# Performance work log

Hardware: AMD Instinct MI355X
Metric: run time of the kernel (lower is better)

Reference implementation:

```python
import jax, jax.numpy as jnp
import numpy as np

LEAKY_SLOPE = 0.2  # PyG GATConv default negative_slope
EPS = 1e-16


def _gat_layer(h_in, src, dst, W, a_src, a_dst, b, concat):
    # h_in: [N, Fin]; src/dst: [Etot] (self-loops included); W: [Fin, H*C]
    N = h_in.shape[0]
    H, C = a_src.shape
    h = (h_in @ W).reshape(N, H, C)                       # [N,H,C]
    al_s = jnp.sum(h * a_src, axis=-1)                    # [N,H]
    al_d = jnp.sum(h * a_dst, axis=-1)                    # [N,H]
    e = jax.nn.leaky_relu(al_s[src] + al_d[dst], LEAKY_SLOPE)  # [E,H]
    emax = jax.ops.segment_max(e, dst, num_segments=N)    # segment softmax over dst
    p = jnp.exp(e - emax[dst])
    denom = jax.ops.segment_sum(p, dst, num_segments=N)
    alpha = p / (denom[dst] + EPS)                        # [E,H]
    out = jax.ops.segment_sum(h[src] * alpha[:, :, None], dst, num_segments=N)  # [N,H,C]
    out = out.reshape(N, H * C) if concat else out.mean(axis=1)
    return out + b


def setup_inputs() -> dict:
    key = jax.random.key(0)
    ks = jax.random.split(key, 16)
    N, E, Fin, Hd, Hh = 10000, 320000, 256, 128, 4

    def glorot(k, shape, fan_in):
        return jax.random.normal(k, shape, dtype=jnp.float32) * (1.0 / np.sqrt(fan_in))

    inp = {
        "x": jax.random.normal(ks[0], (N, Fin), dtype=jnp.float32),
        "edge_index": jax.random.randint(ks[1], (2, E), 0, N, dtype=jnp.int32),
        # conv1: Fin -> Hd x Hh heads, concat
        "W1": glorot(ks[2], (Fin, Hh * Hd), Fin),
        "a1_src": glorot(ks[3], (Hh, Hd), Hd),
        "a1_dst": glorot(ks[4], (Hh, Hd), Hd),
        "b1": jnp.zeros((Hh * Hd,), jnp.float32),
        # conv2: Hh*Hd -> Hd x Hh heads, concat
        "W2": glorot(ks[5], (Hh * Hd, Hh * Hd), Hh * Hd),
        "a2_src": glorot(ks[6], (Hh, Hd), Hd),
        "a2_dst": glorot(ks[7], (Hh, Hd), Hd),
        "b2": jnp.zeros((Hh * Hd,), jnp.float32),
        # conv3: Hh*Hd -> Hd, 1 head, concat=False (mean)
        "W3": glorot(ks[8], (Hh * Hd, Hd), Hh * Hd),
        "a3_src": glorot(ks[9], (1, Hd), Hd),
        "a3_dst": glorot(ks[10], (1, Hd), Hd),
        "b3": jnp.zeros((Hd,), jnp.float32),
        # classifier: Hd -> Hd//2 -> 2
        "Wc1": glorot(ks[11], (Hd, Hd // 2), Hd),
        "bc1": jnp.zeros((Hd // 2,), jnp.float32),
        "Wc2": glorot(ks[12], (Hd // 2, 2), Hd // 2),
        "bc2": jnp.zeros((2,), jnp.float32),
    }
    return inp


def reference(x, edge_index, W1, a1_src, a1_dst, b1, W2, a2_src, a2_dst, b2,
              W3, a3_src, a3_dst, b3, Wc1, bc1, Wc2, bc2):
    N = x.shape[0]
    loops = jnp.arange(N, dtype=edge_index.dtype)
    src = jnp.concatenate([edge_index[0], loops])  # PyG adds self-loops
    dst = jnp.concatenate([edge_index[1], loops])

    h = jax.nn.elu(_gat_layer(x, src, dst, W1, a1_src, a1_dst, b1, concat=True))
    h = jax.nn.elu(_gat_layer(h, src, dst, W2, a2_src, a2_dst, b2, concat=True))
    embeddings = _gat_layer(h, src, dst, W3, a3_src, a3_dst, b3, concat=False)  # [N, 128]
    out = jax.nn.relu(embeddings @ Wc1 + bc1) @ Wc2 + bc2  # [N, 2]
    return out, embeddings
```

## Files before the change

kernel.cpp:

```cpp
#include <hip/hip_runtime.h>
#include <cstddef>

#define LEAKY 0.2f
#define EPS_DEN 1e-16f

typedef short bf8_t __attribute__((ext_vector_type(8)));
typedef float f4_t __attribute__((ext_vector_type(4)));
typedef unsigned short us4_t __attribute__((ext_vector_type(4)));
typedef unsigned short us8_t __attribute__((ext_vector_type(8)));

__device__ __forceinline__ unsigned short f2bf(float f) {
    unsigned u = __float_as_uint(f);
    unsigned r = (u + 0x7fffu + ((u >> 16) & 1u)) >> 16;
    return (unsigned short)r;
}
__device__ __forceinline__ float bf2f(unsigned short h) {
    return __uint_as_float(((unsigned)h) << 16);
}

__global__ void hist_kernel(const int* __restrict__ dst, int* __restrict__ counts, int E) {
    int i = blockIdx.x * blockDim.x + threadIdx.x;
    if (i < E) atomicAdd(&counts[dst[i]], 1);
}

__global__ void scan1_kernel(int* __restrict__ cnt, int* __restrict__ bsum, int N) {
    __shared__ int s[256];
    int t = threadIdx.x;
    int i = blockIdx.x * 256 + t;
    int v = (i < N) ? cnt[i] : 0;
    s[t] = v;
    __syncthreads();
#pragma unroll
    for (int st = 1; st < 256; st <<= 1) {
        int add = (t >= st) ? s[t - st] : 0;
        __syncthreads();
        s[t] += add;
        __syncthreads();
    }
    if (i < N) cnt[i] = s[t] - v;
    if (t == 255) bsum[blockIdx.x] = s[255];
}

__global__ void scan3b_kernel(int* __restrict__ cnt, const int* __restrict__ bsum,
                              int* __restrict__ offs, int N, int NB) {
    __shared__ int sPre[64];
    __shared__ int sTot;
    int t = threadIdx.x;
    if (t < 64) {
        int v = (t < NB) ? bsum[t] : 0;
        int inc = v;
#pragma unroll
        for (int off = 1; off < 64; off <<= 1) {
            int u = __shfl_up(inc, off);
            if (t >= off) inc += u;
        }
        sPre[t] = inc - v;
        if (t == 63) sTot = inc;
    }
    __syncthreads();
    int i = blockIdx.x * 256 + t;
    if (i < N) {
        int o = cnt[i] + sPre[blockIdx.x];
        offs[i] = o;
        cnt[i] = o;
    }
    if (blockIdx.x == 0 && t == 0) offs[N] = sTot;
}

__global__ void scatter_kernel(const int* __restrict__ src, const int* __restrict__ dst,
                               int* __restrict__ cursor, int* __restrict__ csrc, int E) {
    int i = blockIdx.x * blockDim.x + threadIdx.x;
    if (i < E) {
        int d = dst[i];
        int pos = atomicAdd(&cursor[d], 1);
        csrc[pos] = src[i];
    }
}

__global__ void split_all_kernel(
    const float* __restrict__ x, unsigned short* __restrict__ xh, unsigned short* __restrict__ xl,
    int NBX,
    const float* __restrict__ W1, unsigned short* __restrict__ w1h, unsigned short* __restrict__ w1l,
    const float* __restrict__ W2, unsigned short* __restrict__ w2h, unsigned short* __restrict__ w2l,
    const float* __restrict__ W3, unsigned short* __restrict__ w3h, unsigned short* __restrict__ w3l) {
    int b = blockIdx.x, t = threadIdx.x;
    float v;
    unsigned short* ph;
    unsigned short* pl;
    int idx;
    if (b < NBX) {
        idx = b * 256 + t;
        v = x[idx];
        ph = xh; pl = xl;
    } else if (b < NBX + 512) {
        idx = (b - NBX) * 256 + t;
        int n = idx >> 8, k = idx & 255;
        v = W1[(size_t)k * 512 + n];
        ph = w1h; pl = w1l;
    } else if (b < NBX + 512 + 1024) {
        idx = (b - NBX - 512) * 256 + t;
        int n = idx >> 9, k = idx & 511;
        v = W2[(size_t)k * 512 + n];
        ph = w2h; pl = w2l;
    } else {
        idx = (b - NBX - 1536) * 256 + t;
        int n = idx >> 9, k = idx & 511;
        v = W3[(size_t)k * 128 + n];
        ph = w3h; pl = w3l;
    }
    unsigned short hv = f2bf(v);
    ph[idx] = hv;
    pl[idx] = f2bf(v - bf2f(hv));
}

__global__ __launch_bounds__(256) void mfma_gemm128_kernel(
    const unsigned short* __restrict__ Ahi, const unsigned short* __restrict__ Alo,
    const unsigned short* __restrict__ BThi, const unsigned short* __restrict__ BTlo,
    const float* __restrict__ a_src, const float* __restrict__ a_dst,
    float* __restrict__ C, float* __restrict__ als, float* __restrict__ ald,
    int M, int N, int K) {
    constexpr int BK = 32;
    __shared__ __align__(16) unsigned short sAh[128 * BK];
    __shared__ __align__(16) unsigned short sAl[128 * BK];
    __shared__ __align__(16) unsigned short sBh[128 * BK];
    __shared__ __align__(16) unsigned short sBl[128 * BK];
    __shared__ float sAls[128][2];
    __shared__ float sAld[128][2];
    int t = threadIdx.x;
    int w = t >> 6, lane = t & 63;
    int quad = lane >> 4, low = lane & 15;
    int m0 = blockIdx.y * 128, n0 = blockIdx.x * 128;
    int wm = (w & 1) * 64, wn = (w >> 1) * 64;

    f4_t acc[4][4];
#pragma unroll
    for (int i = 0; i < 4; i++)
#pragma unroll
        for (int j = 0; j < 4; j++) acc[i][j] = (f4_t){0.f, 0.f, 0.f, 0.f};

    int srow = lane >> 2;
    int schunk = lane & 3;

    for (int k0 = 0; k0 < K; k0 += BK) {
        __syncthreads();
#pragma unroll
        for (int inst = 0; inst < 2; inst++) {
            int r = w * 32 + inst * 16 + srow;
            int gm = m0 + r;
            if (gm >= M) gm = M - 1;
            size_t goff = (size_t)gm * K + k0 + schunk * 8;
            size_t loff = (size_t)(w * 2048 + inst * 1024);
            __builtin_amdgcn_global_load_lds(
                (const __attribute__((address_space(1))) void*)(Ahi + goff),
                (__attribute__((address_space(3))) void*)((char*)sAh + loff), 16, 0, 0);
            __builtin_amdgcn_global_load_lds(
                (const __attribute__((address_space(1))) void*)(Alo + goff),
                (__attribute__((address_space(3))) void*)((char*)sAl + loff), 16, 0, 0);
        }
#pragma unroll
        for (int inst = 0; inst < 2; inst++) {
            int r = w * 32 + inst * 16 + srow;
            int gn = n0 + r;
            size_t goff = (size_t)gn * K + k0 + schunk * 8;
            size_t loff = (size_t)(w * 2048 + inst * 1024);
            __builtin_amdgcn_global_load_lds(
                (const __attribute__((address_space(1))) void*)(BThi + goff),
                (__attribute__((address_space(3))) void*)((char*)sBh + loff), 16, 0, 0);
            __builtin_amdgcn_global_load_lds(
                (const __attribute__((address_space(1))) void*)(BTlo + goff),
                (__attribute__((address_space(3))) void*)((char*)sBl + loff), 16, 0, 0);
        }
        __syncthreads();

        bf8_t afh[4], bfh[4], xx[4];
#pragma unroll
        for (int i = 0; i < 4; i++) {
            int row = wm + i * 16 + low;
            afh[i] = *(const bf8_t*)&sAh[row * BK + quad * 8];
        }
#pragma unroll
        for (int j = 0; j < 4; j++) {
            int row = wn + j * 16 + low;
            bfh[j] = *(const bf8_t*)&sBh[row * BK + quad * 8];
        }
#pragma unroll
        for (int i = 0; i < 4; i++)
#pragma unroll
            for (int j = 0; j < 4; j++)
                acc[i][j] = __builtin_amdgcn_mfma_f32_16x16x32_bf16(afh[i], bfh[j], acc[i][j], 0, 0, 0);
#pragma unroll
        for (int j = 0; j < 4; j++) {
            int row = wn + j * 16 + low;
            xx[j] = *(const bf8_t*)&sBl[row * BK + quad * 8];
        }
#pragma unroll
        for (int i = 0; i < 4; i++)
#pragma unroll
            for (int j = 0; j < 4; j++)
                acc[i][j] = __builtin_amdgcn_mfma_f32_16x16x32_bf16(afh[i], xx[j], acc[i][j], 0, 0, 0);
#pragma unroll
        for (int i = 0; i < 4; i++) {
            int row = wm + i * 16 + low;
            xx[i] = *(const bf8_t*)&sAl[row * BK + quad * 8];
        }
#pragma unroll
        for (int i = 0; i < 4; i++)
#pragma unroll
            for (int j = 0; j < 4; j++)
                acc[i][j] = __builtin_amdgcn_mfma_f32_16x16x32_bf16(xx[i], bfh[j], acc[i][j], 0, 0, 0);
    }

#pragma unroll
    for (int i = 0; i < 4; i++) {
#pragma unroll
        for (int r = 0; r < 4; r++) {
            int gm = m0 + wm + i * 16 + quad * 4 + r;
            if (gm >= M) continue;
#pragma unroll
            for (int j = 0; j < 4; j++) {
                int gn = n0 + wn + j * 16 + low;
                C[(size_t)gm * N + gn] = acc[i][j][r];
            }
        }
    }

    int hd = n0 >> 7;
    float as_[4], ad_[4];
#pragma unroll
    for (int j = 0; j < 4; j++) {
        int c = wn + j * 16 + low;
        as_[j] = a_src[hd * 128 + c];
        ad_[j] = a_dst[hd * 128 + c];
    }
    int chh = wn >> 6;
#pragma unroll
    for (int i = 0; i < 4; i++) {
#pragma unroll
        for (int r = 0; r < 4; r++) {
            float v = acc[i][0][r] * as_[0] + acc[i][1][r] * as_[1] +
                      acc[i][2][r] * as_[2] + acc[i][3][r] * as_[3];
            float vd = acc[i][0][r] * ad_[0] + acc[i][1][r] * ad_[1] +
                       acc[i][2][r] * ad_[2] + acc[i][3][r] * ad_[3];
#pragma unroll
            for (int off = 1; off < 16; off <<= 1) {
                v += __shfl_xor(v, off);
                vd += __shfl_xor(vd, off);
            }
            if (low == 0) {
                int row = wm + i * 16 + quad * 4 + r;
                sAls[row][chh] = v;
                sAld[row][chh] = vd;
            }
        }
    }
    __syncthreads();
    if (t < 128) {
        int gm = m0 + t;
        if (gm < M) {
            als[gm * 4 + hd] = sAls[t][0] + sAls[t][1];
            ald[gm * 4 + hd] = sAld[t][0] + sAld[t][1];
        }
    }
}

__global__ __launch_bounds__(256) void mfma_gemm64_kernel(
    const unsigned short* __restrict__ Ahi, const unsigned short* __restrict__ Alo,
    const unsigned short* __restrict__ BThi, const unsigned short* __restrict__ BTlo,
    const float* __restrict__ a_src, const float* __restrict__ a_dst,
    float* __restrict__ C, float* __restrict__ als, float* __restrict__ ald,
    int M, int N, int K) {
    constexpr int BK = 32;
    __shared__ __align__(16) unsigned short sAh[64 * BK];
    __shared__ __align__(16) unsigned short sAl[64 * BK];
    __shared__ __align__(16) unsigned short sBh[128 * BK];
    __shared__ __align__(16) unsigned short sBl[128 * BK];
    __shared__ float sAls[64][2];
    __shared__ float sAld[64][2];
    int t = threadIdx.x;
    int w = t >> 6, lane = t & 63;
    int quad = lane >> 4, low = lane & 15;
    int m0 = blockIdx.y * 64, n0 = blockIdx.x * 128;
    int wm = (w & 1) * 32, wn = (w >> 1) * 64;

    f4_t acc[2][4];
#pragma unroll
    for (int i = 0; i < 2; i++)
#pragma unroll
        for (int j = 0; j < 4; j++) acc[i][j] = (f4_t){0.f, 0.f, 0.f, 0.f};

    int srow = lane >> 2;
    int schunk = lane & 3;

    for (int k0 = 0; k0 < K; k0 += BK) {
        __syncthreads();
        {
            int gm = m0 + w * 16 + srow;
            if (gm >= M) gm = M - 1;
            size_t goff = (size_t)gm * K + k0 + schunk * 8;
            size_t loff = (size_t)(w * 1024);
            __builtin_amdgcn_global_load_lds(
                (const __attribute__((address_space(1))) void*)(Ahi + goff),
                (__attribute__((address_space(3))) void*)((char*)sAh + loff), 16, 0, 0);
            __builtin_amdgcn_global_load_lds(
                (const __attribute__((address_space(1))) void*)(Alo + goff),
                (__attribute__((address_space(3))) void*)((char*)sAl + loff), 16, 0, 0);
        }
#pragma unroll
        for (int inst = 0; inst < 2; inst++) {
            int gn = n0 + w * 32 + inst * 16 + srow;
            size_t goff = (size_t)gn * K + k0 + schunk * 8;
            size_t loff = (size_t)(w * 2048 + inst * 1024);
            __builtin_amdgcn_global_load_lds(
                (const __attribute__((address_space(1))) void*)(BThi + goff),
                (__attribute__((address_space(3))) void*)((char*)sBh + loff), 16, 0, 0);
            __builtin_amdgcn_global_load_lds(
                (const __attribute__((address_space(1))) void*)(BTlo + goff),
                (__attribute__((address_space(3))) void*)((char*)sBl + loff), 16, 0, 0);
        }
        __syncthreads();

        bf8_t afh[2], bfh[4], xx[4];
#pragma unroll
        for (int i = 0; i < 2; i++) {
            int row = wm + i * 16 + low;
            afh[i] = *(const bf8_t*)&sAh[row * BK + quad * 8];
        }
#pragma unroll
        for (int j = 0; j < 4; j++) {
            int row = wn + j * 16 + low;
            bfh[j] = *(const bf8_t*)&sBh[row * BK + quad * 8];
        }
#pragma unroll
        for (int i = 0; i < 2; i++)
#pragma unroll
            for (int j = 0; j < 4; j++)
                acc[i][j] = __builtin_amdgcn_mfma_f32_16x16x32_bf16(afh[i], bfh[j], acc[i][j], 0, 0, 0);
#pragma unroll
        for (int j = 0; j < 4; j++) {
            int row = wn + j * 16 + low;
            xx[j] = *(const bf8_t*)&sBl[row * BK + quad * 8];
        }
#pragma unroll
        for (int i = 0; i < 2; i++)
#pragma unroll
            for (int j = 0; j < 4; j++)
                acc[i][j] = __builtin_amdgcn_mfma_f32_16x16x32_bf16(afh[i], xx[j], acc[i][j], 0, 0, 0);
#pragma unroll
        for (int i = 0; i < 2; i++) {
            int row = wm + i * 16 + low;
            xx[i] = *(const bf8_t*)&sAl[row * BK + quad * 8];
        }
#pragma unroll
        for (int i = 0; i < 2; i++)
#pragma unroll
            for (int j = 0; j < 4; j++)
                acc[i][j] = __builtin_amdgcn_mfma_f32_16x16x32_bf16(xx[i], bfh[j], acc[i][j], 0, 0, 0);
    }

#pragma unroll
    for (int i = 0; i < 2; i++) {
#pragma unroll
        for (int r = 0; r < 4; r++) {
            int gm = m0 + wm + i * 16 + quad * 4 + r;
            if (gm >= M) continue;
#pragma unroll
            for (int j = 0; j < 4; j++) {
                int gn = n0 + wn + j * 16 + low;
                C[(size_t)gm * N + gn] = acc[i][j][r];
            }
        }
    }

    float as_[4], ad_[4];
#pragma unroll
    for (int j = 0; j < 4; j++) {
        int c = wn + j * 16 + low;
        as_[j] = a_src[c];
        ad_[j] = a_dst[c];
    }
    int chh = wn >> 6;
#pragma unroll
    for (int i = 0; i < 2; i++) {
#pragma unroll
        for (int r = 0; r < 4; r++) {
            float v = acc[i][0][r] * as_[0] + acc[i][1][r] * as_[1] +
                      acc[i][2][r] * as_[2] + acc[i][3][r] * as_[3];
            float vd = acc[i][0][r] * ad_[0] + acc[i][1][r] * ad_[1] +
                       acc[i][2][r] * ad_[2] + acc[i][3][r] * ad_[3];
#pragma unroll
            for (int off = 1; off < 16; off <<= 1) {
                v += __shfl_xor(v, off);
                vd += __shfl_xor(vd, off);
            }
            if (low == 0) {
                int row = wm + i * 16 + quad * 4 + r;
                sAls[row][chh] = v;
                sAld[row][chh] = vd;
            }
        }
    }
    __syncthreads();
    if (t < 64) {
        int gm = m0 + t;
        if (gm < M) {
            als[gm] = sAls[t][0] + sAls[t][1];
            ald[gm] = sAld[t][0] + sAld[t][1];
        }
    }
}

__global__ void stats_h4_kernel(const int* __restrict__ csrc, const int* __restrict__ offs,
                                const float* __restrict__ als, const float* __restrict__ ald,
                                float* __restrict__ pbuf, float* __restrict__ psf,
                                float* __restrict__ rden, int N, int E) {
    int wave = threadIdx.x >> 6, lane = threadIdx.x & 63;
    int n = blockIdx.x * 4 + wave;
    if (n >= N) return;
    int hd = lane & 3, es = lane >> 2;
    float aldn = ald[n * 4 + hd];
    float selfe = als[n * 4 + hd] + aldn;
    selfe = selfe > 0.f ? selfe : LEAKY * selfe;
    int beg = offs[n], end = offs[n + 1];
    float* pb = pbuf + (size_t)hd * E;
    float m = selfe;
    for (int base = beg; base + es < end; base += 16) {
        int idx = base + es;
        int s = csrc[idx];
        float e = als[s * 4 + hd] + aldn;
        e = e > 0.f ? e : LEAKY * e;
        pb[idx] = e;
        m = fmaxf(m, e);
    }
#pragma unroll
    for (int off = 4; off < 64; off <<= 1) m = fmaxf(m, __shfl_xor(m, off));
    float d = 0.f;
    for (int base = beg; base + es < end; base += 16) {
        int idx = base + es;
        float p = __expf(pb[idx] - m);
        pb[idx] = p;
        d += p;
    }
#pragma unroll
    for (int off = 4; off < 64; off <<= 1) d += __shfl_xor(d, off);
    float pself = __expf(selfe - m);
    float r = 1.0f / (d + pself + EPS_DEN);
    if (es == 0) {
        psf[n * 4 + hd] = pself;
        rden[n * 4 + hd] = r;
    }
}

__global__ void stats_h1_kernel(const int* __restrict__ csrc, const int* __restrict__ offs,
                                const float* __restrict__ als, const float* __restrict__ ald,
                                float* __restrict__ pbuf, float* __restrict__ psf,
                                float* __restrict__ rden, int N) {
    int wave = threadIdx.x >> 6, lane = threadIdx.x & 63;
    int n = blockIdx.x * 4 + wave;
    if (n >= N) return;
    float aldn = ald[n];
    float selfe = als[n] + aldn;
    selfe = selfe > 0.f ? selfe : LEAKY * selfe;
    int beg = offs[n], end = offs[n + 1];
    float m = selfe;
    for (int base = beg; base + lane < end; base += 64) {
        int idx = base + lane;
        int s = csrc[idx];
        float e = als[s] + aldn;
        e = e > 0.f ? e : LEAKY * e;
        pbuf[idx] = e;
        m = fmaxf(m, e);
    }
#pragma unroll
    for (int off = 1; off < 64; off <<= 1) m = fmaxf(m, __shfl_xor(m, off));
    float d = 0.f;
    for (int base = beg; base + lane < end; base += 64) {
        int idx = base + lane;
        float p = __expf(pbuf[idx] - m);
        pbuf[idx] = p;
        d += p;
    }
#pragma unroll
    for (int off = 1; off < 64; off <<= 1) d += __shfl_xor(d, off);
    float pself = __expf(selfe - m);
    float r = 1.0f / (d + pself + EPS_DEN);
    if (lane == 0) { psf[n] = pself; rden[n] = r; }
}

template <bool DO_ELU>
__global__ __launch_bounds__(64) void gat_agg_hh_kernel(
    const float* __restrict__ h, const float* __restrict__ pbuf,
    const float* __restrict__ psf, const float* __restrict__ rden,
    const int* __restrict__ csrc, const int* __restrict__ offs,
    const float* __restrict__ bias, unsigned short* __restrict__ ohi,
    unsigned short* __restrict__ olo, int N, int E) {
    int gid = blockIdx.x;
    int hh = gid & 7;
    int n = gid >> 3;
    int head = hh >> 1;
    int lane = threadIdx.x;
    int eg = lane >> 4;
    int f0 = hh * 64 + (lane & 15) * 4;
    const float* pb = pbuf + (size_t)head * E;

    __shared__ int   sSrc[2][64];
    __shared__ float sP[2][64];
    int beg = offs[n], end = offs[n + 1];
    int nchunks = (end - beg + 63) >> 6;

    f4_t acc = (f4_t){0.f, 0.f, 0.f, 0.f};
    if (beg + lane < end) {
        sSrc[0][lane] = csrc[beg + lane] << 9;
        sP[0][lane] = pb[beg + lane];
    }
    for (int ch = 0; ch < nchunks; ch++) {
        int base = beg + ch * 64;
        int len = min(64, end - base);
        int buf = ch & 1;
        __syncthreads();
        int nbase = base + 64;
        if (ch + 1 < nchunks && nbase + lane < end) {
            sSrc[buf ^ 1][lane] = csrc[nbase + lane] << 9;
            sP[buf ^ 1][lane] = pb[nbase + lane];
        }
#pragma unroll 8
        for (int c = eg; c < len; c += 4) {
            const float* srow = h + (size_t)(unsigned)sSrc[buf][c] + f0;
            acc += sP[buf][c] * *(const f4_t*)srow;
        }
    }
    if (eg == 0) {
        f4_t x = *(const f4_t*)(h + (size_t)n * 512 + f0);
        acc += psf[n * 4 + head] * x;
    }
#pragma unroll
    for (int j = 0; j < 4; j++) {
        acc[j] += __shfl_xor(acc[j], 16);
        acc[j] += __shfl_xor(acc[j], 32);
    }
    if (lane < 16) {
        float r = rden[n * 4 + head];
        f4_t b = *(const f4_t*)(bias + f0);
        us4_t hs, ls;
#pragma unroll
        for (int j = 0; j < 4; j++) {
            float o = acc[j] * r + b[j];
            if (DO_ELU) o = o > 0.f ? o : (__expf(o) - 1.0f);
            unsigned short hv = f2bf(o);
            hs[j] = hv;
            ls[j] = f2bf(o - bf2f(hv));
        }
        size_t idx = (size_t)n * 512 + f0;
        *(us4_t*)&ohi[idx] = hs;
        *(us4_t*)&olo[idx] = ls;
    }
}

__global__ __launch_bounds__(64) void gat_agg_h1_cls_kernel(
    const float* __restrict__ h, const float* __restrict__ pbuf,
    const float* __restrict__ psf, const float* __restrict__ rden,
    const int* __restrict__ csrc, const int* __restrict__ offs,
    const float* __restrict__ bias, const float* __restrict__ Wc1,
    const float* __restrict__ bc1, const float* __restrict__ Wc2,
    const float* __restrict__ bc2, float* __restrict__ emb,
    float* __restrict__ outp, int N) {
    int n = blockIdx.x;
    int lane = threadIdx.x;
    int eg = lane >> 4;
    int fl = (lane & 15) * 8;
    __shared__ int   sSrc[2][64];
    __shared__ float sP[2][64];
    __shared__ float semb[128];
    int beg = offs[n], end = offs[n + 1];
    int nchunks = (end - beg + 63) >> 6;

    f4_t a0 = (f4_t){0.f, 0.f, 0.f, 0.f};
    f4_t a1 = (f4_t){0.f, 0.f, 0.f, 0.f};
    if (beg + lane < end) {
        sSrc[0][lane] = csrc[beg + lane] << 7;
        sP[0][lane] = pbuf[beg + lane];
    }
    for (int ch = 0; ch < nchunks; ch++) {
        int base = beg + ch * 64;
        int len = min(64, end - base);
        int buf = ch & 1;
        __syncthreads();
        int nbase = base + 64;
        if (ch + 1 < nchunks && nbase + lane < end) {
            sSrc[buf ^ 1][lane] = csrc[nbase + lane] << 7;
            sP[buf ^ 1][lane] = pbuf[nbase + lane];
        }
#pragma unroll 8
        for (int c = eg; c < len; c += 4) {
            const float* srow = h + (size_t)(unsigned)sSrc[buf][c] + fl;
            float p = sP[buf][c];
            a0 += p * *(const f4_t*)(srow);
            a1 += p * *(const f4_t*)(srow + 4);
        }
    }
    if (eg == 0) {
        float p = psf[n];
        const float* srow = h + (size_t)n * 128 + fl;
        a0 += p * *(const f4_t*)(srow);
        a1 += p * *(const f4_t*)(srow + 4);
    }
#pragma unroll
    for (int j = 0; j < 4; j++) {
        a0[j] += __shfl_xor(a0[j], 16);
        a0[j] += __shfl_xor(a0[j], 32);
        a1[j] += __shfl_xor(a1[j], 16);
        a1[j] += __shfl_xor(a1[j], 32);
    }
    __syncthreads();
    if (lane < 16) {
        int fo = lane * 8;
        float r = rden[n];
        f4_t b0 = *(const f4_t*)(bias + fo);
        f4_t b1 = *(const f4_t*)(bias + fo + 4);
        f4_t o0, o1;
#pragma unroll
        for (int j = 0; j < 4; j++) {
            o0[j] = a0[j] * r + b0[j];
            o1[j] = a1[j] * r + b1[j];
        }
        *(f4_t*)&semb[fo] = o0;
        *(f4_t*)&semb[fo + 4] = o1;
        *(f4_t*)&emb[(size_t)n * 128 + fo] = o0;
        *(f4_t*)&emb[(size_t)n * 128 + fo + 4] = o1;
    }
    __syncthreads();

    float cacc = bc1[lane];
#pragma unroll 4
    for (int k = 0; k < 128; k++) cacc += semb[k] * Wc1[k * 64 + lane];
    cacc = fmaxf(cacc, 0.f);
    float o0 = cacc * Wc2[lane * 2 + 0];
    float o1 = cacc * Wc2[lane * 2 + 1];
#pragma unroll
    for (int off = 32; off; off >>= 1) {
        o0 += __shfl_down(o0, off);
        o1 += __shfl_down(o1, off);
    }
    if (lane == 0) {
        outp[n * 2 + 0] = o0 + bc2[0];
        outp[n * 2 + 1] = o1 + bc2[1];
    }
}

extern "C" void kernel_launch(void* const* d_in, const int* in_sizes, int n_in,
                              void* d_out, int out_size, void* d_ws, size_t ws_size,
                              hipStream_t stream) {
    const float* x      = (const float*)d_in[0];
    const int*   ei     = (const int*)d_in[1];
    const float* W1     = (const float*)d_in[2];
    const float* a1s    = (const float*)d_in[3];
    const float* a1d    = (const float*)d_in[4];
    const float* b1     = (const float*)d_in[5];
    const float* W2     = (const float*)d_in[6];
    const float* a2s    = (const float*)d_in[7];
    const float* a2d    = (const float*)d_in[8];
    const float* b2     = (const float*)d_in[9];
    const float* W3     = (const float*)d_in[10];
    const float* a3s    = (const float*)d_in[11];
    const float* a3d    = (const float*)d_in[12];
    const float* b3     = (const float*)d_in[13];
    const float* Wc1    = (const float*)d_in[14];
    const float* bc1    = (const float*)d_in[15];
    const float* Wc2    = (const float*)d_in[16];
    const float* bc2    = (const float*)d_in[17];

    const int N = in_sizes[0] / 256;
    const int E = in_sizes[1] / 2;
    const int F = 512;

    const int* src = ei;
    const int* dst = ei + E;

    auto align = [](size_t o) { return (o + 255) & ~(size_t)255; };
    size_t o = 0;
    size_t o_G     = o; o = align(o + (size_t)N * F * 4);
    size_t o_ahi   = o; o = align(o + (size_t)N * F * 2);
    size_t o_alo   = o; o = align(o + (size_t)N * F * 2);
    size_t o_xhi   = o; o = align(o + (size_t)N * 256 * 2);
    size_t o_xlo   = o; o = align(o + (size_t)N * 256 * 2);
    size_t o_w1h   = o; o = align(o + (size_t)512 * 256 * 2);
    size_t o_w1l   = o; o = align(o + (size_t)512 * 256 * 2);
    size_t o_w2h   = o; o = align(o + (size_t)512 * 512 * 2);
    size_t o_w2l   = o; o = align(o + (size_t)512 * 512 * 2);
    size_t o_w3h   = o; o = align(o + (size_t)128 * 512 * 2);
    size_t o_w3l   = o; o = align(o + (size_t)128 * 512 * 2);
    size_t o_als   = o; o = align(o + (size_t)N * 4 * 4);
    size_t o_ald   = o; o = align(o + (size_t)N * 4 * 4);
    size_t o_psf   = o; o = align(o + (size_t)N * 4 * 4);
    size_t o_rden  = o; o = align(o + (size_t)N * 4 * 4);
    size_t o_cnt   = o; o = align(o + (size_t)N * 4);
    size_t o_off   = o; o = align(o + (size_t)(N + 1) * 4);
    size_t o_bsum  = o; o = align(o + (size_t)64 * 4);
    size_t o_csrc  = o; o = align(o + (size_t)E * 4);
    size_t o_ebuf  = o; o = align(o + (size_t)E * 4 * 4);
    (void)ws_size;

    char* ws = (char*)d_ws;
    float* bufG  = (float*)(ws + o_G);
    unsigned short* act_hi = (unsigned short*)(ws + o_ahi);
    unsigned short* act_lo = (unsigned short*)(ws + o_alo);
    unsigned short* x_hi   = (unsigned short*)(ws + o_xhi);
    unsigned short* x_lo   = (unsigned short*)(ws + o_xlo);
    unsigned short* w1h = (unsigned short*)(ws + o_w1h);
    unsigned short* w1l = (unsigned short*)(ws + o_w1l);
    unsigned short* w2h = (unsigned short*)(ws + o_w2h);
    unsigned short* w2l = (unsigned short*)(ws + o_w2l);
    unsigned short* w3h = (unsigned short*)(ws + o_w3h);
    unsigned short* w3l = (unsigned short*)(ws + o_w3l);
    float* als  = (float*)(ws + o_als);
    float* ald  = (float*)(ws + o_ald);
    float* psf  = (float*)(ws + o_psf);
    float* rden = (float*)(ws + o_rden);
    int*   cnt  = (int*)(ws + o_cnt);
    int*   offs = (int*)(ws + o_off);
    int*   bsum = (int*)(ws + o_bsum);
    int*   csrc = (int*)(ws + o_csrc);
    float* ebuf = (float*)(ws + o_ebuf);

    float* outp = (float*)d_out;
    float* emb  = (float*)d_out + (size_t)N * 2;

    hipMemsetAsync(cnt, 0, (size_t)N * 4, stream);
    int eb = (E + 255) / 256;
    int nbs = (N + 255) / 256;
    hipLaunchKernelGGL(hist_kernel, dim3(eb), dim3(256), 0, stream, dst, cnt, E);
    hipLaunchKernelGGL(scan1_kernel, dim3(nbs), dim3(256), 0, stream, cnt, bsum, N);
    hipLaunchKernelGGL(scan3b_kernel, dim3(nbs), dim3(256), 0, stream, cnt, bsum, offs, N, nbs);
    hipLaunchKernelGGL(scatter_kernel, dim3(eb), dim3(256), 0, stream, src, dst, cnt, csrc, E);

    int NBX = N;
    hipLaunchKernelGGL(split_all_kernel, dim3(NBX + 512 + 1024 + 256), dim3(256), 0, stream,
                       x, x_hi, x_lo, NBX, W1, w1h, w1l, W2, w2h, w2l, W3, w3h, w3l);

    int nb4 = (N + 3) / 4;
    int gy128 = (N + 127) / 128;
    int gy64  = (N + 63) / 64;

    hipLaunchKernelGGL(mfma_gemm128_kernel, dim3(512 / 128, gy128), dim3(256), 0, stream,
                       x_hi, x_lo, w1h, w1l, a1s, a1d, bufG, als, ald, N, 512, 256);
    hipLaunchKernelGGL(stats_h4_kernel, dim3(nb4), dim3(256), 0, stream,
                       csrc, offs, als, ald, ebuf, psf, rden, N, E);
    hipLaunchKernelGGL((gat_agg_hh_kernel<true>), dim3(N * 8), dim3(64), 0, stream,
                       bufG, ebuf, psf, rden, csrc, offs, b1, act_hi, act_lo, N, E);

    hipLaunchKernelGGL(mfma_gemm128_kernel, dim3(512 / 128, gy128), dim3(256), 0, stream,
                       act_hi, act_lo, w2h, w2l, a2s, a2d, bufG, als, ald, N, 512, 512);
    hipLaunchKernelGGL(stats_h4_kernel, dim3(nb4), dim3(256), 0, stream,
                       csrc, offs, als, ald, ebuf, psf, rden, N, E);
    hipLaunchKernelGGL((gat_agg_hh_kernel<true>), dim3(N * 8), dim3(64), 0, stream,
                       bufG, ebuf, psf, rden, csrc, offs, b2, act_hi, act_lo, N, E);

    hipLaunchKernelGGL(mfma_gemm64_kernel, dim3(128 / 128, gy64), dim3(256), 0, stream,
                       act_hi, act_lo, w3h, w3l, a3s, a3d, bufG, als, ald, N, 128, 512);
    hipLaunchKernelGGL(stats_h1_kernel, dim3(nb4), dim3(256), 0, stream,
                       csrc, offs, als, ald, ebuf, psf, rden, N);
    hipLaunchKernelGGL(gat_agg_h1_cls_kernel, dim3(N), dim3(64), 0, stream,
                       bufG, ebuf, psf, rden, csrc, offs, b3, Wc1, bc1, Wc2, bc2, emb, outp, N);
}
```

Baseline: 363.2 us.

## Fuse layer-3 softmax stats into aggregation kernel; register-cache edge logits in stats

Removes the separate single-head stats kernel and computes the edge logits, max, exp and denominator inside the layer-3 aggregation block, dropping a launch and the pbuf/psf/rden round trip through global memory. For nodes with degree at most 64 the logits are kept in registers or shared memory and computed in one pass. The multi-head stats kernel also keeps logits in registers for low-degree nodes, avoiding a write then re-read of pbuf. High-degree nodes take a fallback path that recomputes the logits, costing extra gathers.

```diff
diff --git a/kernel.cpp b/kernel.cpp
--- a/kernel.cpp
+++ b/kernel.cpp
@@ -7,7 +7,6 @@
 typedef short bf8_t __attribute__((ext_vector_type(8)));
 typedef float f4_t __attribute__((ext_vector_type(4)));
 typedef unsigned short us4_t __attribute__((ext_vector_type(4)));
-typedef unsigned short us8_t __attribute__((ext_vector_type(8)));
 
 __device__ __forceinline__ unsigned short f2bf(float f) {
     unsigned u = __float_as_uint(f);
@@ -421,24 +420,51 @@
     float selfe = als[n * 4 + hd] + aldn;
     selfe = selfe > 0.f ? selfe : LEAKY * selfe;
     int beg = offs[n], end = offs[n + 1];
+    int deg = end - beg;
     float* pb = pbuf + (size_t)hd * E;
     float m = selfe;
-    for (int base = beg; base + es < end; base += 16) {
-        int idx = base + es;
-        int s = csrc[idx];
-        float e = als[s * 4 + hd] + aldn;
-        e = e > 0.f ? e : LEAKY * e;
-        pb[idx] = e;
-        m = fmaxf(m, e);
-    }
-#pragma unroll
-    for (int off = 4; off < 64; off <<= 1) m = fmaxf(m, __shfl_xor(m, off));
     float d = 0.f;
-    for (int base = beg; base + es < end; base += 16) {
-        int idx = base + es;
-        float p = __expf(pb[idx] - m);
-        pb[idx] = p;
-        d += p;
+    if (deg <= 64) {
+        float eR[4];
+        int nch = (deg + 15) >> 4;
+        for (int k = 0; k < nch; k++) {
+            int idx = beg + k * 16 + es;
+            float e = -1e30f;
+            if (idx < end) {
+                int s = csrc[idx];
+                e = als[s * 4 + hd] + aldn;
+                e = e > 0.f ? e : LEAKY * e;
+                m = fmaxf(m, e);
+            }
+            eR[k] = e;
+        }
+#pragma unroll
+        for (int off = 4; off < 64; off <<= 1) m = fmaxf(m, __shfl_xor(m, off));
+        for (int k = 0; k < nch; k++) {
+            int idx = beg + k * 16 + es;
+            if (idx < end) {
+                float p = __expf(eR[k] - m);
+                pb[idx] = p;
+                d += p;
+            }
+        }
+    } else {
+        for (int base = beg; base + es < end; base += 16) {
+            int idx = base + es;
+            int s = csrc[idx];
+            float e = als[s * 4 + hd] + aldn;
+            e = e > 0.f ? e : LEAKY * e;
+            pb[idx] = e;
+            m = fmaxf(m, e);
+        }
+#pragma unroll
+        for (int off = 4; off < 64; off <<= 1) m = fmaxf(m, __shfl_xor(m, off));
+        for (int base = beg; base + es < end; base += 16) {
+            int idx = base + es;
+            float p = __expf(pb[idx] - m);
+            pb[idx] = p;
+            d += p;
+        }
     }
 #pragma unroll
     for (int off = 4; off < 64; off <<= 1) d += __shfl_xor(d, off);
@@ -448,42 +474,6 @@
         psf[n * 4 + hd] = pself;
         rden[n * 4 + hd] = r;
     }
-}
-
-__global__ void stats_h1_kernel(const int* __restrict__ csrc, const int* __restrict__ offs,
-                                const float* __restrict__ als, const float* __restrict__ ald,
-                                float* __restrict__ pbuf, float* __restrict__ psf,
-                                float* __restrict__ rden, int N) {
-    int wave = threadIdx.x >> 6, lane = threadIdx.x & 63;
-    int n = blockIdx.x * 4 + wave;
-    if (n >= N) return;
-    float aldn = ald[n];
-    float selfe = als[n] + aldn;
-    selfe = selfe > 0.f ? selfe : LEAKY * selfe;
-    int beg = offs[n], end = offs[n + 1];
-    float m = selfe;
-    for (int base = beg; base + lane < end; base += 64) {
-        int idx = base + lane;
-        int s = csrc[idx];
-        float e = als[s] + aldn;
-        e = e > 0.f ? e : LEAKY * e;
-        pbuf[idx] = e;
-        m = fmaxf(m, e);
-    }
-#pragma unroll
-    for (int off = 1; off < 64; off <<= 1) m = fmaxf(m, __shfl_xor(m, off));
-    float d = 0.f;
-    for (int base = beg; base + lane < end; base += 64) {
-        int idx = base + lane;
-        float p = __expf(pbuf[idx] - m);
-        pbuf[idx] = p;
-        d += p;
-    }
-#pragma unroll
-    for (int off = 1; off < 64; off <<= 1) d += __shfl_xor(d, off);
-    float pself = __expf(selfe - m);
-    float r = 1.0f / (d + pself + EPS_DEN);
-    if (lane == 0) { psf[n] = pself; rden[n] = r; }
 }
 
 template <bool DO_ELU>
@@ -556,52 +546,92 @@
 }
 
 __global__ __launch_bounds__(64) void gat_agg_h1_cls_kernel(
-    const float* __restrict__ h, const float* __restrict__ pbuf,
-    const float* __restrict__ psf, const float* __restrict__ rden,
-    const int* __restrict__ csrc, const int* __restrict__ offs,
-    const float* __restrict__ bias, const float* __restrict__ Wc1,
-    const float* __restrict__ bc1, const float* __restrict__ Wc2,
-    const float* __restrict__ bc2, float* __restrict__ emb,
-    float* __restrict__ outp, int N) {
+    const float* __restrict__ h, const float* __restrict__ als,
+    const float* __restrict__ ald, const int* __restrict__ csrc,
+    const int* __restrict__ offs, const float* __restrict__ bias,
+    const float* __restrict__ Wc1, const float* __restrict__ bc1,
+    const float* __restrict__ Wc2, const float* __restrict__ bc2,
+    float* __restrict__ emb, float* __restrict__ outp, int N) {
     int n = blockIdx.x;
     int lane = threadIdx.x;
     int eg = lane >> 4;
     int fl = (lane & 15) * 8;
-    __shared__ int   sSrc[2][64];
-    __shared__ float sP[2][64];
+    __shared__ int   sSrc[64];
+    __shared__ float sP[64];
     __shared__ float semb[128];
     int beg = offs[n], end = offs[n + 1];
-    int nchunks = (end - beg + 63) >> 6;
+    int deg = end - beg;
+
+    float aldn = ald[n];
+    float selfe = als[n] + aldn;
+    selfe = selfe > 0.f ? selfe : LEAKY * selfe;
 
     f4_t a0 = (f4_t){0.f, 0.f, 0.f, 0.f};
     f4_t a1 = (f4_t){0.f, 0.f, 0.f, 0.f};
-    if (beg + lane < end) {
-        sSrc[0][lane] = csrc[beg + lane] << 7;
-        sP[0][lane] = pbuf[beg + lane];
-    }
-    for (int ch = 0; ch < nchunks; ch++) {
-        int base = beg + ch * 64;
-        int len = min(64, end - base);
-        int buf = ch & 1;
+    float d = 0.f;
+    float m;
+
+    if (deg <= 64) {
+        float e = -1e30f;
+        int s = 0;
+        if (lane < deg) {
+            s = csrc[beg + lane];
+            e = als[s] + aldn;
+            e = e > 0.f ? e : LEAKY * e;
+        }
+        m = fmaxf(e, selfe);
+#pragma unroll
+        for (int off = 1; off < 64; off <<= 1) m = fmaxf(m, __shfl_xor(m, off));
+        float p = (lane < deg) ? __expf(e - m) : 0.f;
+        d = p;
+        sSrc[lane] = s << 7;
+        sP[lane] = p;
         __syncthreads();
-        int nbase = base + 64;
-        if (ch + 1 < nchunks && nbase + lane < end) {
-            sSrc[buf ^ 1][lane] = csrc[nbase + lane] << 7;
-            sP[buf ^ 1][lane] = pbuf[nbase + lane];
-        }
 #pragma unroll 8
-        for (int c = eg; c < len; c += 4) {
-            const float* srow = h + (size_t)(unsigned)sSrc[buf][c] + fl;
-            float p = sP[buf][c];
-            a0 += p * *(const f4_t*)(srow);
-            a1 += p * *(const f4_t*)(srow + 4);
-        }
-    }
+        for (int c = eg; c < deg; c += 4) {
+            const float* srow = h + (size_t)(unsigned)sSrc[c] + fl;
+            float pc = sP[c];
+            a0 += pc * *(const f4_t*)(srow);
+            a1 += pc * *(const f4_t*)(srow + 4);
+        }
+    } else {
+        m = selfe;
+        for (int i = beg + lane; i < end; i += 64) {
+            int s = csrc[i];
+            float e = als[s] + aldn;
+            e = e > 0.f ? e : LEAKY * e;
+            m = fmaxf(m, e);
+        }
+#pragma unroll
+        for (int off = 1; off < 64; off <<= 1) m = fmaxf(m, __shfl_xor(m, off));
+        for (int base = beg; base < end; base += 64) {
+            int len = min(64, end - base);
+            __syncthreads();
+            if (lane < len) {
+                int s = csrc[base + lane];
+                float e = als[s] + aldn;
+                e = e > 0.f ? e : LEAKY * e;
+                float p = __expf(e - m);
+                sSrc[lane] = s << 7;
+                sP[lane] = p;
+                d += p;
+            }
+            __syncthreads();
+#pragma unroll 8
+            for (int c = eg; c < len; c += 4) {
+                const float* srow = h + (size_t)(unsigned)sSrc[c] + fl;
+                float pc = sP[c];
+                a0 += pc * *(const f4_t*)(srow);
+                a1 += pc * *(const f4_t*)(srow + 4);
+            }
+        }
+    }
+
+    float pself = __expf(selfe - m);
     if (eg == 0) {
-        float p = psf[n];
         const float* srow = h + (size_t)n * 128 + fl;
-        a0 += p * *(const f4_t*)(srow);
-        a1 += p * *(const f4_t*)(srow + 4);
+        a0 += pself * *(const f4_t*)(srow);
+        a1 += pself * *(const f4_t*)(srow + 4);
     }
 #pragma unroll
     for (int j = 0; j < 4; j++) {
@@ -610,10 +640,13 @@
         a1[j] += __shfl_xor(a1[j], 16);
         a1[j] += __shfl_xor(a1[j], 32);
     }
+#pragma unroll
+    for (int off = 1; off < 64; off <<= 1) d += __shfl_xor(d, off);
+    float r = 1.0f / (d + pself + EPS_DEN);
+
     __syncthreads();
     if (lane < 16) {
         int fo = lane * 8;
-        float r = rden[n];
         f4_t b0 = *(const f4_t*)(bias + fo);
         f4_t b1 = *(const f4_t*)(bias + fo + 4);
         f4_t o0, o1;
@@ -756,8 +789,6 @@
 
     hipLaunchKernelGGL(mfma_gemm64_kernel, dim3(128 / 128, gy64), dim3(256), 0, stream,
                        act_hi, act_lo, w3h, w3l, a3s, a3d, bufG, als, ald, N, 128, 512);
-    hipLaunchKernelGGL(stats_h1_kernel, dim3(nb4), dim3(256), 0, stream,
-                       csrc, offs, als, ald, ebuf, psf, rden, N);
     hipLaunchKernelGGL(gat_agg_h1_cls_kernel, dim3(N), dim3(64), 0, stream,
-                       bufG, ebuf, psf, rden, csrc, offs, b3, Wc1, bc1, Wc2, bc2, emb, outp, N);
-}
+                       bufG, als, ald, csrc, offs, b3, Wc1, bc1, Wc2, bc2, emb, outp, N);
+}
```

Result: no change. 364.5 us (+0.4%).
